# Kernel tuning notes

Hardware: AMD Instinct MI355X
Metric: run time of the kernel (lower is better)

## Reference

```python
import jax, jax.numpy as jnp
import numpy as np

B, C, H, W = 8, 64, 256, 256


def setup_inputs() -> dict:
    key = jax.random.key(0)
    k1, k2, k3 = jax.random.split(key, 3)
    phi = jax.random.normal(k1, (B, 2, H, W), dtype=jnp.float32) * 2.0
    x_enc = jax.random.normal(k2, (B, C, H, W), dtype=jnp.float32)
    m = jax.random.uniform(k3, (B, 1, H, W), dtype=jnp.float32)
    return {"phi": phi, "x_enc": x_enc, "m": m}


def _grid_sample_bilinear_zeros(x, grid):
    """torch.nn.functional.grid_sample defaults: bilinear, zeros padding,
    align_corners=False. x: [b,c,h,w], grid: [b,h,w,2] in [-1,1] (x,y order)."""
    b, c, h, w = x.shape
    # unnormalize (align_corners=False convention)
    ix = (grid[..., 0] + 1.0) * (0.5 * w) - 0.5  # [b,h,w]
    iy = (grid[..., 1] + 1.0) * (0.5 * h) - 0.5
    x0 = jnp.floor(ix)
    y0 = jnp.floor(iy)
    x1 = x0 + 1.0
    y1 = y0 + 1.0
    wx1 = ix - x0
    wx0 = 1.0 - wx1
    wy1 = iy - y0
    wy0 = 1.0 - wy1

    bidx = jnp.arange(b)[:, None, None]

    def corner(yy, xx, wgt):
        valid = (xx >= 0) & (xx < w) & (yy >= 0) & (yy < h)
        xc = jnp.clip(xx, 0, w - 1).astype(jnp.int32)
        yc = jnp.clip(yy, 0, h - 1).astype(jnp.int32)
        v = x[bidx, :, yc, xc]  # gather -> [b,h,w,c]
        return v * (wgt * valid.astype(x.dtype))[..., None]

    out = (corner(y0, x0, wy0 * wx0) + corner(y0, x1, wy0 * wx1)
           + corner(y1, x0, wy1 * wx0) + corner(y1, x1, wy1 * wx1))  # [b,h,w,c]
    return jnp.transpose(out, (0, 3, 1, 2))  # [b,c,h,w]


def reference(phi, x_enc, m):
    b, c, h, w = x_enc.shape
    # pixel coordinate grid: channel 0 = x (width), channel 1 = y (height)
    yy, xx = jnp.meshgrid(jnp.arange(h, dtype=jnp.float32),
                          jnp.arange(w, dtype=jnp.float32), indexing="ij")
    grid = jnp.stack([xx, yy], axis=0)[None]  # [1,2,h,w]
    vgrid = grid + phi                         # [b,2,h,w]
    vx = 2.0 * vgrid[:, 0] / max(w - 1, 1) - 1.0
    vy = 2.0 * vgrid[:, 1] / max(h - 1, 1) - 1.0
    vgrid = jnp.stack([vx, vy], axis=-1)       # [b,h,w,2]
    # original: phi = phi.permute(0,2,3,1); vgrid = vgrid + 2*phi
    vgrid = vgrid + 2.0 * jnp.transpose(phi, (0, 2, 3, 1))
    out = _grid_sample_bilinear_zeros(x_enc, vgrid)
    return out * m
```

## Files before the change

kernel.cpp:

```cpp
#include <hip/hip_runtime.h>

namespace {

constexpr int B = 8, C = 64, H = 256, W = 256;
constexpr int HW = H * W;
constexpr int TP = 64;
constexpr int TSTRIDE = 68;

typedef float v4f __attribute__((ext_vector_type(4)));

__global__ __launch_bounds__(256) void warp_kernel(
    const float* __restrict__ phi,
    const float* __restrict__ xenc,
    const float* __restrict__ mm,
    float* __restrict__ out)
{
    __shared__ float tile[64 * TSTRIDE];
    __shared__ float s_w[4][TP];
    __shared__ int   s_o[4][TP];
    __shared__ int   s_p[TP];
    __shared__ int   s_n;

    const int t   = threadIdx.x;
    const int bid = blockIdx.x;
    const int wt  = bid & 3;
    const int h   = (bid >> 2) & (H - 1);
    const int b   = bid >> 10;
    const int w0  = wt * 64;

    {
        v4f z = {0.f, 0.f, 0.f, 0.f};
        for (int i = t; i < (64 * TSTRIDE) / 4; i += 256)
            *(v4f*)&tile[i * 4] = z;
    }

    if (t < 64) {
        const int lane = t;
        const int w    = w0 + lane;
        const int hw   = h * W + w;

        const float p0 = phi[(size_t)(b * 2 + 0) * HW + hw];
        const float p1 = phi[(size_t)(b * 2 + 1) * HW + hw];
        const float mv = mm[(size_t)b * HW + hw];

        const float gx = (2.0f * ((float)w + p0)) / (float)(W - 1) - 1.0f + 2.0f * p0;
        const float gy = (2.0f * ((float)h + p1)) / (float)(H - 1) - 1.0f + 2.0f * p1;
        const float ix = (gx + 1.0f) * (0.5f * (float)W) - 0.5f;
        const float iy = (gy + 1.0f) * (0.5f * (float)H) - 0.5f;

        const float x0f = floorf(ix);
        const float y0f = floorf(iy);
        const float fx1 = ix - x0f, fx0 = 1.0f - fx1;
        const float fy1 = iy - y0f, fy0 = 1.0f - fy1;

        const float wm1 = (float)(W - 1), hm1 = (float)(H - 1);
        const int x0 = (int)fminf(fmaxf(x0f,        0.0f), wm1);
        const int x1 = (int)fminf(fmaxf(x0f + 1.0f, 0.0f), wm1);
        const int y0 = (int)fminf(fmaxf(y0f,        0.0f), hm1);
        const int y1 = (int)fminf(fmaxf(y0f + 1.0f, 0.0f), hm1);

        const bool vx0 = (x0f >= 0.0f) && (x0f < (float)W);
        const bool vx1 = (x0f + 1.0f >= 0.0f) && (x0f + 1.0f < (float)W);
        const bool vy0 = (y0f >= 0.0f) && (y0f < (float)H);
        const bool vy1 = (y0f + 1.0f >= 0.0f) && (y0f + 1.0f < (float)H);

        const float w00 = fy0 * fx0 * ((vy0 && vx0) ? mv : 0.0f);
        const float w01 = fy0 * fx1 * ((vy0 && vx1) ? mv : 0.0f);
        const float w10 = fy1 * fx0 * ((vy1 && vx0) ? mv : 0.0f);
        const float w11 = fy1 * fx1 * ((vy1 && vx1) ? mv : 0.0f);

        const bool inb = (w00 + w01 + w10 + w11) != 0.0f;

        const unsigned long long mask = __ballot(inb);
        const int pos = __popcll(mask & ((1ULL << lane) - 1ULL));
        if (inb) {
            s_w[0][pos] = w00;  s_w[1][pos] = w01;
            s_w[2][pos] = w10;  s_w[3][pos] = w11;
            s_o[0][pos] = y0 * W + x0;
            s_o[1][pos] = y0 * W + x1;
            s_o[2][pos] = y1 * W + x0;
            s_o[3][pos] = y1 * W + x1;
            s_p[pos]    = lane;
        }
        if (lane == 0) s_n = __popcll(mask);
    }
    __syncthreads();

    {
        const int wv   = t >> 6;
        const int lane = t & 63;
        const int n    = s_n;
        const float* __restrict__ xb = xenc + ((size_t)b * C + lane) * HW;
        for (int i = wv; i < n; i += 4) {
            const float w00 = s_w[0][i], w01 = s_w[1][i];
            const float w10 = s_w[2][i], w11 = s_w[3][i];
            const int o00 = s_o[0][i], o01 = s_o[1][i];
            const int o10 = s_o[2][i], o11 = s_o[3][i];
            const int p   = s_p[i];
            const float v = xb[o00] * w00 + xb[o01] * w01
                          + xb[o10] * w10 + xb[o11] * w11;
            tile[lane * TSTRIDE + p] = v;
        }
    }
    __syncthreads();

    {
        const size_t obase = (size_t)b * C * HW + (size_t)h * W + w0;
        const int cl = t >> 4;
        const int p4 = (t & 15) * 4;
        #pragma unroll
        for (int pass = 0; pass < 4; ++pass) {
            const int c = pass * 16 + cl;
            v4f v = *(const v4f*)&tile[c * TSTRIDE + p4];
            __builtin_nontemporal_store(v, (v4f*)(out + obase + (size_t)c * HW + p4));
        }
    }
}

}

extern "C" void kernel_launch(void* const* d_in, const int* in_sizes, int n_in,
                              void* d_out, int out_size, void* d_ws, size_t ws_size,
                              hipStream_t stream) {
    const float* phi  = (const float*)d_in[0];
    const float* xenc = (const float*)d_in[1];
    const float* mm   = (const float*)d_in[2];
    float* out = (float*)d_out;

    const int blocks = B * H * (W / 64);
    warp_kernel<<<dim3(blocks), dim3(256), 0, stream>>>(phi, xenc, mm, out);
}
```

Before: 243.8 us.

## Pre-transpose input to channels-last fp16 for coalesced bilinear gathers

Adds a transpose kernel that converts x_enc from NCHW fp32 to NHWC fp16 in the workspace. The warp kernel then gathers each corner's 64 channels as one contiguous 128-byte row instead of 64 strided plane accesses. This aims to remove uncoalesced scattered reads, at the cost of an extra pass over the input and fp16 rounding of input values. It falls back to the old kernel if the workspace is too small.

```diff
diff --git a/kernel.cpp b/kernel.cpp
--- a/kernel.cpp
+++ b/kernel.cpp
@@ -8,6 +8,172 @@
 constexpr int TSTRIDE = 68;
 
 typedef float v4f __attribute__((ext_vector_type(4)));
+typedef _Float16 h2 __attribute__((ext_vector_type(2)));
+typedef _Float16 h8 __attribute__((ext_vector_type(8)));
+
+__global__ __launch_bounds__(256) void transpose_kernel(
+    const float* __restrict__ xenc, _Float16* __restrict__ xt)
+{
+    __shared__ float lds[64 * 68];
+    const int t   = threadIdx.x;
+    const int bid = blockIdx.x;
+    const int b   = bid >> 10;
+    const int hw0 = (bid & 1023) << 6;
+
+    {
+        const int k  = t & 15;
+        const int cr = t >> 4;
+        #pragma unroll
+        for (int r = 0; r < 4; ++r) {
+            const int c = r * 16 + cr;
+            const v4f v = __builtin_nontemporal_load(
+                (const v4f*)(xenc + (((size_t)(b * C + c)) << 16) + hw0 + k * 4));
+            #pragma unroll
+            for (int e = 0; e < 4; ++e)
+                lds[(k * 4 + e) * 68 + c] = v[e];
+        }
+    }
+    __syncthreads();
+    {
+        const int p  = t >> 2;
+        const int c0 = (t & 3) * 16;
+        float f[16];
+        #pragma unroll
+        for (int j = 0; j < 4; ++j) {
+            const v4f v = *(const v4f*)(lds + p * 68 + c0 + 4 * j);
+            f[4 * j + 0] = v[0]; f[4 * j + 1] = v[1];
+            f[4 * j + 2] = v[2]; f[4 * j + 3] = v[3];
+        }
+        h8 o0, o1;
+        #pragma unroll
+        for (int i = 0; i < 8; ++i) {
+            o0[i] = (_Float16)f[i];
+            o1[i] = (_Float16)f[8 + i];
+        }
+        _Float16* dst = xt + (((size_t)(b * HW + hw0 + p)) << 6) + c0;
+        __builtin_nontemporal_store(o0, (h8*)dst);
+        __builtin_nontemporal_store(o1, (h8*)(dst + 8));
+    }
+}
+
+__global__ __launch_bounds__(256) void warp2_kernel(
+    const float* __restrict__ phi,
+    const _Float16* __restrict__ xt,
+    const float* __restrict__ mm,
+    float* __restrict__ out)
+{
+    __shared__ float tile[64 * TSTRIDE];
+    __shared__ float s_w[4][TP];
+    __shared__ int   s_o[4][TP];
+    __shared__ int   s_p[TP];
+    __shared__ int   s_n;
+
+    const int t   = threadIdx.x;
+    const int bid = blockIdx.x;
+    const int wt  = bid & 3;
+    const int h   = (bid >> 2) & (H - 1);
+    const int b   = bid >> 10;
+    const int w0  = wt * 64;
+
+    {
+        v4f z = {0.f, 0.f, 0.f, 0.f};
+        for (int i = t; i < (64 * TSTRIDE) / 4; i += 256)
+            *(v4f*)&tile[i * 4] = z;
+    }
+
+    if (t < 64) {
+        const int lane = t;
+        const int w    = w0 + lane;
+        const int hw   = h * W + w;
+
+        const float p0 = phi[(size_t)(b * 2 + 0) * HW + hw];
+        const float p1 = phi[(size_t)(b * 2 + 1) * HW + hw];
+        const float mv = mm[(size_t)b * HW + hw];
+
+        const float gx = (2.0f * ((float)w + p0)) / (float)(W - 1) - 1.0f + 2.0f * p0;
+        const float gy = (2.0f * ((float)h + p1)) / (float)(H - 1) - 1.0f + 2.0f * p1;
+        const float ix = (gx + 1.0f) * (0.5f * (float)W) - 0.5f;
+        const float iy = (gy + 1.0f) * (0.5f * (float)H) - 0.5f;
+
+        const float x0f = floorf(ix);
+        const float y0f = floorf(iy);
+        const float fx1 = ix - x0f, fx0 = 1.0f - fx1;
+        const float fy1 = iy - y0f, fy0 = 1.0f - fy1;
+
+        const float wm1 = (float)(W - 1), hm1 = (float)(H - 1);
+        const int x0 = (int)fminf(fmaxf(x0f,        0.0f), wm1);
+        const int x1 = (int)fminf(fmaxf(x0f + 1.0f, 0.0f), wm1);
+        const int y0 = (int)fminf(fmaxf(y0f,        0.0f), hm1);
+        const int y1 = (int)fminf(fmaxf(y0f + 1.0f, 0.0f), hm1);
+
+        const bool vx0 = (x0f >= 0.0f) && (x0f < (float)W);
+        const bool vx1 = (x0f + 1.0f >= 0.0f) && (x0f + 1.0f < (float)W);
+        const bool vy0 = (y0f >= 0.0f) && (y0f < (float)H);
+        const bool vy1 = (y0f + 1.0f >= 0.0f) && (y0f + 1.0f < (float)H);
+
+        const float w00 = fy0 * fx0 * ((vy0 && vx0) ? mv : 0.0f);
+        const float w01 = fy0 * fx1 * ((vy0 && vx1) ? mv : 0.0f);
+        const float w10 = fy1 * fx0 * ((vy1 && vx0) ? mv : 0.0f);
+        const float w11 = fy1 * fx1 * ((vy1 && vx1) ? mv : 0.0f);
+
+        const bool inb = (w00 + w01 + w10 + w11) != 0.0f;
+
+        const unsigned long long mask = __ballot(inb);
+        const int pos = __popcll(mask & ((1ULL << lane) - 1ULL));
+        if (inb) {
+            s_w[0][pos] = w00;  s_w[1][pos] = w01;
+            s_w[2][pos] = w10;  s_w[3][pos] = w11;
+            s_o[0][pos] = y0 * W + x0;
+            s_o[1][pos] = y0 * W + x1;
+            s_o[2][pos] = y1 * W + x0;
+            s_o[3][pos] = y1 * W + x1;
+            s_p[pos]    = lane;
+        }
+        if (lane == 0) s_n = __popcll(mask);
+    }
+    __syncthreads();
+
+    {
+        const int wv   = t >> 6;
+        const int lane = t & 63;
+        const int sub  = lane >> 5;
+        const int k    = lane & 31;
+        const int n    = s_n;
+        const _Float16* __restrict__ xtb = xt + ((size_t)b << 22);
+
+        for (int i0 = wv * 2; i0 < n; i0 += 8) {
+            const int i = i0 + sub;
+            if (i < n) {
+                const float w00 = s_w[0][i], w01 = s_w[1][i];
+                const float w10 = s_w[2][i], w11 = s_w[3][i];
+                const h2 v00 = *(const h2*)(xtb + (((size_t)s_o[0][i]) << 6) + 2 * k);
+                const h2 v01 = *(const h2*)(xtb + (((size_t)s_o[1][i]) << 6) + 2 * k);
+                const h2 v10 = *(const h2*)(xtb + (((size_t)s_o[2][i]) << 6) + 2 * k);
+                const h2 v11 = *(const h2*)(xtb + (((size_t)s_o[3][i]) << 6) + 2 * k);
+                const float lo = (float)v00[0] * w00 + (float)v01[0] * w01
+                               + (float)v10[0] * w10 + (float)v11[0] * w11;
+                const float hi = (float)v00[1] * w00 + (float)v01[1] * w01
+                               + (float)v10[1] * w10 + (float)v11[1] * w11;
+                const int p = s_p[i];
+                tile[(2 * k    ) * TSTRIDE + p] = lo;
+                tile[(2 * k + 1) * TSTRIDE + p] = hi;
+            }
+        }
+    }
+    __syncthreads();
+
+    {
+        const size_t obase = (size_t)b * C * HW + (size_t)h * W + w0;
+        const int cl = t >> 4;
+        const int p4 = (t & 15) * 4;
+        #pragma unroll
+        for (int pass = 0; pass < 4; ++pass) {
+            const int c = pass * 16 + cl;
+            v4f v = *(const v4f*)&tile[c * TSTRIDE + p4];
+            __builtin_nontemporal_store(v, (v4f*)(out + obase + (size_t)c * HW + p4));
+        }
+    }
+}
 
 __global__ __launch_bounds__(256) void warp_kernel(
     const float* __restrict__ phi,
@@ -128,5 +294,13 @@
     float* out = (float*)d_out;
 
     const int blocks = B * H * (W / 64);
-    warp_kernel<<<dim3(blocks), dim3(256), 0, stream>>>(phi, xenc, mm, out);
-}
+    const size_t xt_bytes = (size_t)B * C * HW * sizeof(_Float16);
+
+    if (d_ws != nullptr && ws_size >= xt_bytes) {
+        _Float16* xt = (_Float16*)d_ws;
+        transpose_kernel<<<dim3(blocks), dim3(256), 0, stream>>>(xenc, xt);
+        warp2_kernel<<<dim3(blocks), dim3(256), 0, stream>>>(phi, xt, mm, out);
+    } else {
+        warp_kernel<<<dim3(blocks), dim3(256), 0, stream>>>(phi, xenc, mm, out);
+    }
+}
```

Result: slower. 253.5 us (+4.0%).
